# Kernel optimization log

Measured on AMD Instinct MI355X. Metric: run time of the kernel, lower is better.

Reference implementation:

```python
import jax, jax.numpy as jnp
import numpy as np

EPS = 1e-5      # batch-norm epsilon
ALPHA = 0.2     # leaky_relu negative slope


def bn_lrelu(h, gamma, beta):
    # training-mode batch norm over the batch axis, then leaky relu
    mean = jnp.mean(h, axis=0)
    var = jnp.var(h, axis=0)
    h = (h - mean) * jax.lax.rsqrt(var + EPS) * gamma + beta
    return jnp.where(h >= 0, h, ALPHA * h)


def setup_inputs() -> dict:
    key = jax.random.key(0)
    ks = jax.random.split(key, 16)
    O, T, Din, H, Dout = 50000, 200000, 128, 512, 128
    s = 0.02
    inp = {
        "obj_vecs": jax.random.normal(ks[0], (O, Din), jnp.float32),
        "pred_vecs": jax.random.normal(ks[1], (T, Din), jnp.float32),
        "edges": jax.random.randint(ks[2], (T, 2), 0, O, jnp.int64),
        # net1: [3*Din -> H -> 2H+Dout], each Linear followed by BN + leaky_relu
        "W1a": jax.random.normal(ks[3], (3 * Din, H), jnp.float32) * s,
        "b1a": jnp.zeros((H,), jnp.float32),
        "g1a": jnp.ones((H,), jnp.float32),
        "be1a": jnp.zeros((H,), jnp.float32),
        "W1b": jax.random.normal(ks[4], (H, 2 * H + Dout), jnp.float32) * s,
        "b1b": jnp.zeros((2 * H + Dout,), jnp.float32),
        "g1b": jnp.ones((2 * H + Dout,), jnp.float32),
        "be1b": jnp.zeros((2 * H + Dout,), jnp.float32),
        # net2: [H -> H -> Dout]
        "W2a": jax.random.normal(ks[5], (H, H), jnp.float32) * s,
        "b2a": jnp.zeros((H,), jnp.float32),
        "g2a": jnp.ones((H,), jnp.float32),
        "be2a": jnp.zeros((H,), jnp.float32),
        "W2b": jax.random.normal(ks[6], (H, Dout), jnp.float32) * s,
        "b2b": jnp.zeros((Dout,), jnp.float32),
        "g2b": jnp.ones((Dout,), jnp.float32),
        "be2b": jnp.zeros((Dout,), jnp.float32),
    }
    return inp


def reference(obj_vecs, pred_vecs, edges,
              W1a, b1a, g1a, be1a, W1b, b1b, g1b, be1b,
              W2a, b2a, g2a, be2a, W2b, b2b, g2b, be2b):
    O = obj_vecs.shape[0]
    H = W1a.shape[1]
    Dout = W2b.shape[1]
    s_idx = edges[:, 0]
    o_idx = edges[:, 1]

    # gather subject/object vecs and concat with predicate vecs: [T, 3*Din]
    cur_t = jnp.concatenate([obj_vecs[s_idx], pred_vecs, obj_vecs[o_idx]], axis=1)

    # net1 MLP
    h = bn_lrelu(cur_t @ W1a + b1a, g1a, be1a)           # [T, H]
    new_t = bn_lrelu(h @ W1b + b1b, g1b, be1b)            # [T, 2H+Dout]

    new_s = new_t[:, :H]
    new_p = new_t[:, H:H + Dout]
    new_o = new_t[:, H + Dout:]

    # scatter-add pooling back to objects, then average
    pooled = jnp.zeros((O, H), jnp.float32).at[s_idx].add(new_s).at[o_idx].add(new_o)
    counts = jnp.zeros((O,), jnp.float32).at[s_idx].add(1.0).at[o_idx].add(1.0)
    counts = jnp.clip(counts, 1.0, float(O))
    pooled = pooled / counts[:, None]

    # net2 MLP
    h2 = bn_lrelu(pooled @ W2a + b2a, g2a, be2a)          # [O, H]
    new_obj = bn_lrelu(h2 @ W2b + b2b, g2b, be2b)         # [O, Dout]
    return new_obj, new_p
```

## Files before the change

kernel.cpp:

```cpp
#include <hip/hip_runtime.h>

typedef __bf16 bf16;
typedef __bf16 bf16x8 __attribute__((ext_vector_type(8)));
typedef float  f32x4  __attribute__((ext_vector_type(4)));

#define BM 128
#define BN 128
#define BKT 64
#define LDK (BKT + 8)

template<int AMODE, int EPI>
__global__ __launch_bounds__(256) void gemm_k(
    const bf16* __restrict__ Abf, const float* __restrict__ Af32,
    const float* __restrict__ obj, const float* __restrict__ pred,
    const int* __restrict__ edges, const float* __restrict__ invcnt,
    const float* __restrict__ scale, const float* __restrict__ shift,
    const float* __restrict__ oscale, const float* __restrict__ oshift,
    const bf16* __restrict__ WT,
    bf16* __restrict__ outB, float* __restrict__ outF,
    float* __restrict__ pooled, float* __restrict__ gsum, float* __restrict__ gsq,
    int M, int N, int K)
{
  __shared__ __align__(16) bf16 As[BM][LDK];
  __shared__ __align__(16) bf16 Bs[BN][LDK];
  __shared__ float sc_sh[512];
  __shared__ float sh_sh[512];
  __shared__ float osc[BN];
  __shared__ float osh[BN];
  __shared__ int eS[BM];
  __shared__ int eO[BM];

  const int tid = threadIdx.x;
  const int m0 = blockIdx.x * BM;
  const int n0 = blockIdx.y * BN;
  const int lane = tid & 63;
  const int w = tid >> 6;
  const int wm = (w >> 1) * 64;
  const int wn = (w & 1) * 64;
  const int l15 = lane & 15;
  const int quad = lane >> 4;

  if (AMODE == 1) {
    for (int c = tid; c < K; c += 256) { sc_sh[c] = scale[c]; sh_sh[c] = shift[c]; }
  }
  if (EPI == 2) {
    if (tid < BN) { osc[tid] = oscale[n0 + tid]; osh[tid] = oshift[n0 + tid]; }
  }
  if (AMODE == 0 || EPI == 2) {
    if (tid < BM) {
      int r = m0 + tid; if (r >= M) r = M - 1;
      eS[tid] = edges[2 * r];
      eO[tid] = edges[2 * r + 1];
    }
  }
  __syncthreads();

  f32x4 acc[4][4];
  #pragma unroll
  for (int i = 0; i < 4; ++i)
    #pragma unroll
    for (int j = 0; j < 4; ++j)
      acc[i][j] = (f32x4){0.f, 0.f, 0.f, 0.f};

  for (int k0 = 0; k0 < K; k0 += BKT) {
    {
      int idx = tid;
      #pragma unroll
      for (int it = 0; it < 4; ++it, idx += 256) {
        int r = idx >> 3, c8 = (idx & 7) << 3;
        bf16x8 v = *reinterpret_cast<const bf16x8*>(WT + (size_t)(n0 + r) * K + k0 + c8);
        *reinterpret_cast<bf16x8*>(&Bs[r][c8]) = v;
      }
    }
    if (AMODE == 1) {
      int idx = tid;
      #pragma unroll
      for (int it = 0; it < 4; ++it, idx += 256) {
        int r = idx >> 3, c8 = (idx & 7) << 3;
        int row = m0 + r; if (row >= M) row = M - 1;
        bf16x8 v = *reinterpret_cast<const bf16x8*>(Abf + (size_t)row * K + k0 + c8);
        bf16x8 o;
        #pragma unroll
        for (int e = 0; e < 8; ++e) {
          int c = k0 + c8 + e;
          float f = sc_sh[c] * (float)v[e] + sh_sh[c];
          f = f >= 0.f ? f : 0.2f * f;
          o[e] = (bf16)f;
        }
        *reinterpret_cast<bf16x8*>(&As[r][c8]) = o;
      }
    } else {
      int idx = tid;
      #pragma unroll
      for (int it = 0; it < 8; ++it, idx += 256) {
        int r = idx >> 4, c4 = (idx & 15) << 2;
        int row = m0 + r; if (row >= M) row = M - 1;
        const float* src;
        float mul = 1.f;
        if (AMODE == 0) {
          int k = k0 + c4;
          if (k < 128)      src = obj  + (size_t)eS[r] * 128 + k;
          else if (k < 256) src = pred + (size_t)row * 128 + (k - 128);
          else              src = obj  + (size_t)eO[r] * 128 + (k - 256);
        } else {
          src = Af32 + (size_t)row * K + k0 + c4;
          mul = invcnt[row];
        }
        float4 v = *reinterpret_cast<const float4*>(src);
        As[r][c4 + 0] = (bf16)(v.x * mul);
        As[r][c4 + 1] = (bf16)(v.y * mul);
        As[r][c4 + 2] = (bf16)(v.z * mul);
        As[r][c4 + 3] = (bf16)(v.w * mul);
      }
    }
    __syncthreads();
    #pragma unroll
    for (int kk = 0; kk < BKT; kk += 32) {
      bf16x8 af[4], bfv[4];
      #pragma unroll
      for (int i = 0; i < 4; ++i)
        af[i] = *reinterpret_cast<const bf16x8*>(&As[wm + i * 16 + l15][kk + quad * 8]);
      #pragma unroll
      for (int j = 0; j < 4; ++j)
        bfv[j] = *reinterpret_cast<const bf16x8*>(&Bs[wn + j * 16 + l15][kk + quad * 8]);
      #pragma unroll
      for (int i = 0; i < 4; ++i)
        #pragma unroll
        for (int j = 0; j < 4; ++j)
          acc[i][j] = __builtin_amdgcn_mfma_f32_16x16x32_bf16(af[i], bfv[j], acc[i][j], 0, 0, 0);
    }
    __syncthreads();
  }

  if (EPI == 2) {
    #pragma unroll
    for (int i = 0; i < 4; ++i) {
      #pragma unroll
      for (int r = 0; r < 4; ++r) {
        int lrow = wm + i * 16 + quad * 4 + r;
        int row = m0 + lrow;
        if (row >= M) continue;
        #pragma unroll
        for (int j = 0; j < 4; ++j) {
          int cl = wn + j * 16 + l15;
          int n1 = n0 + cl;
          float v = osc[cl] * acc[i][j][r] + osh[cl];
          v = v >= 0.f ? v : 0.2f * v;
          if (n1 < 512)      atomicAdd(&pooled[(size_t)eS[lrow] * 512 + n1], v);
          else if (n1 < 640) outF[(size_t)row * 128 + (n1 - 512)] = v;
          else               atomicAdd(&pooled[(size_t)eO[lrow] * 512 + (n1 - 640)], v);
        }
      }
    }
  } else {
    #pragma unroll
    for (int j = 0; j < 4; ++j) {
      float s = 0.f, q = 0.f;
      #pragma unroll
      for (int i = 0; i < 4; ++i) {
        #pragma unroll
        for (int r = 0; r < 4; ++r) {
          int row = m0 + wm + i * 16 + quad * 4 + r;
          if (row >= M) continue;
          float v = acc[i][j][r];
          s += v; q += v * v;
          int col = n0 + wn + j * 16 + l15;
          if (EPI == 0) outB[(size_t)row * N + col] = (bf16)v;
          if (EPI == 3) outF[(size_t)row * N + col] = v;
        }
      }
      s += __shfl_xor(s, 16); q += __shfl_xor(q, 16);
      s += __shfl_xor(s, 32); q += __shfl_xor(q, 32);
      if (quad == 0) {
        int col = n0 + wn + j * 16 + l15;
        atomicAdd(&gsum[col], s);
        atomicAdd(&gsq[col], q);
      }
    }
  }
}

__global__ __launch_bounds__(256) void tconv_k(const float* __restrict__ W,
                                               bf16* __restrict__ WT, int K, int N) {
  int idx = blockIdx.x * 256 + threadIdx.x;
  if (idx < K * N) {
    int n = idx / K, k = idx - n * K;
    WT[(size_t)n * K + k] = (bf16)W[(size_t)k * N + n];
  }
}

__global__ __launch_bounds__(256) void bnfin_k(const float* __restrict__ sum,
    const float* __restrict__ sq, const float* __restrict__ g,
    const float* __restrict__ be, float* __restrict__ scale,
    float* __restrict__ shift, int C, float invR) {
  int c = blockIdx.x * 256 + threadIdx.x;
  if (c < C) {
    float m = sum[c] * invR;
    float v = sq[c] * invR - m * m;
    float a = g[c] * rsqrtf(v + 1e-5f);
    scale[c] = a;
    shift[c] = be[c] - m * a;
  }
}

__global__ __launch_bounds__(256) void counts_k(const int* __restrict__ edges,
                                                float* __restrict__ counts, int T) {
  int t = blockIdx.x * 256 + threadIdx.x;
  if (t < T) {
    atomicAdd(&counts[edges[2 * t]], 1.f);
    atomicAdd(&counts[edges[2 * t + 1]], 1.f);
  }
}

__global__ __launch_bounds__(256) void invcnt_k(float* __restrict__ counts, int O) {
  int i = blockIdx.x * 256 + threadIdx.x;
  if (i < O) {
    float c = counts[i];
    c = fminf(fmaxf(c, 1.f), (float)O);
    counts[i] = 1.f / c;
  }
}

__global__ __launch_bounds__(256) void final_k(float* __restrict__ buf,
    const float* __restrict__ scale, const float* __restrict__ shift, int n) {
  int i = blockIdx.x * 256 + threadIdx.x;
  if (i < n) {
    int c = i & 127;
    float v = scale[c] * buf[i] + shift[c];
    buf[i] = v >= 0.f ? v : 0.2f * v;
  }
}

extern "C" void kernel_launch(void* const* d_in, const int* in_sizes, int n_in,
                              void* d_out, int out_size, void* d_ws, size_t ws_size,
                              hipStream_t stream) {
  const float* obj   = (const float*)d_in[0];
  const float* pred  = (const float*)d_in[1];
  const int*   edges = (const int*)d_in[2];
  const float* W1a = (const float*)d_in[3];
  const float* g1a = (const float*)d_in[5];
  const float* be1a= (const float*)d_in[6];
  const float* W1b = (const float*)d_in[7];
  const float* g1b = (const float*)d_in[9];
  const float* be1b= (const float*)d_in[10];
  const float* W2a = (const float*)d_in[11];
  const float* g2a = (const float*)d_in[13];
  const float* be2a= (const float*)d_in[14];
  const float* W2b = (const float*)d_in[15];
  const float* g2b = (const float*)d_in[17];
  const float* be2b= (const float*)d_in[18];

  const int O = in_sizes[0] / 128;
  const int T = in_sizes[1] / 128;
  float* out_obj = (float*)d_out;
  float* out_p   = (float*)d_out + (size_t)O * 128;

  char* base = (char*)d_ws;
  size_t off = 0;
  auto alloc = [&](size_t bytes) { size_t p = off; off += (bytes + 255) & ~(size_t)255; return p; };
  size_t oWT1a = alloc((size_t)384 * 512 * 2);
  size_t oWT1b = alloc((size_t)512 * 1152 * 2);
  size_t oWT2a = alloc((size_t)512 * 512 * 2);
  size_t oWT2b = alloc((size_t)512 * 128 * 2);
  size_t oSums = alloc(4608 * 4);
  size_t oScl  = alloc(4608 * 4);
  size_t oCnt  = alloc((size_t)O * 4);
  size_t oHA   = alloc((size_t)T * 512 * 2);
  size_t oPool = alloc((size_t)O * 512 * 4);

  bf16* WT1a = (bf16*)(base + oWT1a);
  bf16* WT1b = (bf16*)(base + oWT1b);
  bf16* WT2a = (bf16*)(base + oWT2a);
  bf16* WT2b = (bf16*)(base + oWT2b);
  float* sums = (float*)(base + oSums);
  float* sumA = sums,        * sqA = sums + 512;
  float* sumB = sums + 1024, * sqB = sums + 2176;
  float* sumC = sums + 3328, * sqC = sums + 3840;
  float* sumD = sums + 4352, * sqD = sums + 4480;
  float* scl = (float*)(base + oScl);
  float* scaleA = scl,        * shiftA = scl + 512;
  float* scaleB = scl + 1024, * shiftB = scl + 2176;
  float* scaleC = scl + 3328, * shiftC = scl + 3840;
  float* scaleD = scl + 4352, * shiftD = scl + 4480;
  float* counts = (float*)(base + oCnt);
  bf16*  hA = (bf16*)(base + oHA);
  bf16*  h2 = (bf16*)(base + oHA);
  float* pooled = (float*)(base + oPool);
  float* objpre = out_obj;

  hipMemsetAsync(sums, 0, 4608 * 4, stream);
  hipMemsetAsync(counts, 0, (size_t)O * 4, stream);
  hipMemsetAsync(pooled, 0, (size_t)O * 512 * 4, stream);

  tconv_k<<<(384 * 512 + 255) / 256, 256, 0, stream>>>(W1a, WT1a, 384, 512);
  tconv_k<<<(512 * 1152 + 255) / 256, 256, 0, stream>>>(W1b, WT1b, 512, 1152);
  tconv_k<<<(512 * 512 + 255) / 256, 256, 0, stream>>>(W2a, WT2a, 512, 512);
  tconv_k<<<(512 * 128 + 255) / 256, 256, 0, stream>>>(W2b, WT2b, 512, 128);
  counts_k<<<(T + 255) / 256, 256, 0, stream>>>(edges, counts, T);
  invcnt_k<<<(O + 255) / 256, 256, 0, stream>>>(counts, O);

  {
    dim3 g((T + BM - 1) / BM, 512 / BN);
    gemm_k<0, 0><<<g, 256, 0, stream>>>(nullptr, nullptr, obj, pred, edges, nullptr,
        nullptr, nullptr, nullptr, nullptr, WT1a, hA, nullptr, nullptr, sumA, sqA,
        T, 512, 384);
  }
  bnfin_k<<<2, 256, 0, stream>>>(sumA, sqA, g1a, be1a, scaleA, shiftA, 512, 1.f / T);

  {
    dim3 g((T + BM - 1) / BM, 1152 / BN);
    gemm_k<1, 1><<<g, 256, 0, stream>>>(hA, nullptr, nullptr, nullptr, nullptr, nullptr,
        scaleA, shiftA, nullptr, nullptr, WT1b, nullptr, nullptr, nullptr, sumB, sqB,
        T, 1152, 512);
  }
  bnfin_k<<<5, 256, 0, stream>>>(sumB, sqB, g1b, be1b, scaleB, shiftB, 1152, 1.f / T);

  {
    dim3 g((T + BM - 1) / BM, 1152 / BN);
    gemm_k<1, 2><<<g, 256, 0, stream>>>(hA, nullptr, nullptr, nullptr, edges, nullptr,
        scaleA, shiftA, scaleB, shiftB, WT1b, nullptr, out_p, pooled, nullptr, nullptr,
        T, 1152, 512);
  }

  {
    dim3 g((O + BM - 1) / BM, 512 / BN);
    gemm_k<2, 0><<<g, 256, 0, stream>>>(nullptr, pooled, nullptr, nullptr, nullptr, counts,
        nullptr, nullptr, nullptr, nullptr, WT2a, h2, nullptr, nullptr, sumC, sqC,
        O, 512, 512);
  }
  bnfin_k<<<2, 256, 0, stream>>>(sumC, sqC, g2a, be2a, scaleC, shiftC, 512, 1.f / O);

  {
    dim3 g((O + BM - 1) / BM, 128 / BN);
    gemm_k<1, 3><<<g, 256, 0, stream>>>(h2, nullptr, nullptr, nullptr, nullptr, nullptr,
        scaleC, shiftC, nullptr, nullptr, WT2b, nullptr, objpre, nullptr, sumD, sqD,
        O, 128, 512);
  }
  bnfin_k<<<1, 256, 0, stream>>>(sumD, sqD, g2b, be2b, scaleD, shiftD, 128, 1.f / O);

  final_k<<<((size_t)O * 128 + 255) / 256, 256, 0, stream>>>(objpre, scaleD, shiftD,
      (int)((size_t)O * 128));
}
```

Before: 2.208 ms.

## Store pre-BN second GEMM output and replace atomic scatter with CSR gather pooling

Instead of running the 1152-wide net1 second GEMM twice (once for BN stats, once to recompute and atomically scatter into pooled), the GEMM runs once and stores the pre-activation output as bf16. A CSR adjacency is then built with an int count, a single-block scan and a fill pass, and a gather kernel applies BN plus leaky relu and averages the contributions per object into a bf16 pooled buffer. The first BN activation is applied once in place by a standalone kernel. This removes a full large GEMM and the float atomics, at the cost of extra global traffic for the T x 1152 bf16 staging buffer, extra bf16 rounding of pooled, and a fallback path used when the workspace is too small.

```diff
diff --git a/kernel.cpp b/kernel.cpp
--- a/kernel.cpp
+++ b/kernel.cpp
@@ -23,12 +23,12 @@
 {
   __shared__ __align__(16) bf16 As[BM][LDK];
   __shared__ __align__(16) bf16 Bs[BN][LDK];
-  __shared__ float sc_sh[512];
-  __shared__ float sh_sh[512];
-  __shared__ float osc[BN];
-  __shared__ float osh[BN];
-  __shared__ int eS[BM];
-  __shared__ int eO[BM];
+  __shared__ float sc_sh[(AMODE == 1) ? 512 : 1];
+  __shared__ float sh_sh[(AMODE == 1) ? 512 : 1];
+  __shared__ float osc[(EPI == 2) ? BN : 1];
+  __shared__ float osh[(EPI == 2) ? BN : 1];
+  __shared__ int eS[(AMODE == 0 || EPI == 2) ? BM : 1];
+  __shared__ int eO[(AMODE == 0 || EPI == 2) ? BM : 1];
 
   const int tid = threadIdx.x;
   const int m0 = blockIdx.x * BM;
@@ -72,22 +72,26 @@
         *reinterpret_cast<bf16x8*>(&Bs[r][c8]) = v;
       }
     }
-    if (AMODE == 1) {
+    if (AMODE == 1 || AMODE == 3) {
       int idx = tid;
       #pragma unroll
       for (int it = 0; it < 4; ++it, idx += 256) {
         int r = idx >> 3, c8 = (idx & 7) << 3;
         int row = m0 + r; if (row >= M) row = M - 1;
         bf16x8 v = *reinterpret_cast<const bf16x8*>(Abf + (size_t)row * K + k0 + c8);
-        bf16x8 o;
-        #pragma unroll
-        for (int e = 0; e < 8; ++e) {
-          int c = k0 + c8 + e;
-          float f = sc_sh[c] * (float)v[e] + sh_sh[c];
-          f = f >= 0.f ? f : 0.2f * f;
-          o[e] = (bf16)f;
+        if (AMODE == 1) {
+          bf16x8 o;
+          #pragma unroll
+          for (int e = 0; e < 8; ++e) {
+            int c = k0 + c8 + e;
+            float f = sc_sh[c] * (float)v[e] + sh_sh[c];
+            f = f >= 0.f ? f : 0.2f * f;
+            o[e] = (bf16)f;
+          }
+          *reinterpret_cast<bf16x8*>(&As[r][c8]) = o;
+        } else {
+          *reinterpret_cast<bf16x8*>(&As[r][c8]) = v;
         }
-        *reinterpret_cast<bf16x8*>(&As[r][c8]) = o;
       }
     } else {
       int idx = tid;
@@ -203,22 +207,133 @@
   }
 }
 
-__global__ __launch_bounds__(256) void counts_k(const int* __restrict__ edges,
-                                                float* __restrict__ counts, int T) {
+__global__ __launch_bounds__(256) void cntint_k(const int* __restrict__ edges,
+                                                int* __restrict__ cnt, int T) {
   int t = blockIdx.x * 256 + threadIdx.x;
   if (t < T) {
-    atomicAdd(&counts[edges[2 * t]], 1.f);
-    atomicAdd(&counts[edges[2 * t + 1]], 1.f);
-  }
-}
-
-__global__ __launch_bounds__(256) void invcnt_k(float* __restrict__ counts, int O) {
+    atomicAdd(&cnt[edges[2 * t]], 1);
+    atomicAdd(&cnt[edges[2 * t + 1]], 1);
+  }
+}
+
+__global__ __launch_bounds__(256) void invcnt_k(const int* __restrict__ cnt,
+                                                float* __restrict__ invc, int O) {
   int i = blockIdx.x * 256 + threadIdx.x;
   if (i < O) {
-    float c = counts[i];
-    c = fminf(fmaxf(c, 1.f), (float)O);
-    counts[i] = 1.f / c;
-  }
+    float c = fminf(fmaxf((float)cnt[i], 1.f), (float)O);
+    invc[i] = 1.f / c;
+  }
+}
+
+__global__ __launch_bounds__(1024) void scan_k(const int* __restrict__ cnt,
+    int* __restrict__ rowptr, int* __restrict__ head, int O, int total) {
+  __shared__ int sh[1024];
+  const int t = threadIdx.x;
+  const int C = (O + 1023) / 1024;
+  const int i0 = t * C;
+  int s = 0;
+  for (int i = 0; i < C; ++i) { int idx = i0 + i; if (idx < O) s += cnt[idx]; }
+  sh[t] = s;
+  __syncthreads();
+  for (int d = 1; d < 1024; d <<= 1) {
+    int v = (t >= d) ? sh[t - d] : 0;
+    __syncthreads();
+    sh[t] += v;
+    __syncthreads();
+  }
+  int run = (t == 0) ? 0 : sh[t - 1];
+  for (int i = 0; i < C; ++i) {
+    int idx = i0 + i;
+    if (idx < O) { rowptr[idx] = run; head[idx] = run; run += cnt[idx]; }
+  }
+  if (t == 0) rowptr[O] = total;
+}
+
+__global__ __launch_bounds__(256) void fill_k(const int* __restrict__ edges,
+    int* __restrict__ head, int* __restrict__ list, int T) {
+  int t = blockIdx.x * 256 + threadIdx.x;
+  if (t < T) {
+    int s = edges[2 * t];
+    int p = atomicAdd(&head[s], 1);
+    list[p] = t << 1;
+    int o = edges[2 * t + 1];
+    p = atomicAdd(&head[o], 1);
+    list[p] = (t << 1) | 1;
+  }
+}
+
+__global__ __launch_bounds__(256) void act_k(bf16* __restrict__ hA,
+    const float* __restrict__ scale, const float* __restrict__ shift, size_t n8) {
+  size_t i = (size_t)blockIdx.x * 256 + threadIdx.x;
+  if (i < n8) {
+    size_t idx8 = i * 8;
+    int c = (int)(idx8 & 511);
+    bf16x8 v = *reinterpret_cast<const bf16x8*>(hA + idx8);
+    bf16x8 o;
+    #pragma unroll
+    for (int j = 0; j < 8; ++j) {
+      float f = scale[c + j] * (float)v[j] + shift[c + j];
+      f = f >= 0.f ? f : 0.2f * f;
+      o[j] = (bf16)f;
+    }
+    *reinterpret_cast<bf16x8*>(hA + idx8) = o;
+  }
+}
+
+__global__ __launch_bounds__(256) void newp_k(const bf16* __restrict__ tB,
+    const float* __restrict__ scale, const float* __restrict__ shift,
+    float* __restrict__ outP, int T) {
+  int i = blockIdx.x * 256 + threadIdx.x;
+  if (i < T * 128) {
+    int t = i >> 7, c = i & 127;
+    float v = scale[512 + c] * (float)tB[(size_t)t * 1152 + 512 + c] + shift[512 + c];
+    outP[i] = v >= 0.f ? v : 0.2f * v;
+  }
+}
+
+__global__ __launch_bounds__(256) void gather_k(const bf16* __restrict__ tB,
+    const int* __restrict__ rowptr, const int* __restrict__ list,
+    const float* __restrict__ scale, const float* __restrict__ shift,
+    const float* __restrict__ invc, bf16* __restrict__ pooled, int O) {
+  int o = blockIdx.x * 4 + (threadIdx.x >> 6);
+  if (o >= O) return;
+  int lane = threadIdx.x & 63;
+  int c0 = lane * 8;
+  float scS[8], shS[8], scO[8], shO[8];
+  #pragma unroll
+  for (int j = 0; j < 8; ++j) {
+    scS[j] = scale[c0 + j];       shS[j] = shift[c0 + j];
+    scO[j] = scale[640 + c0 + j]; shO[j] = shift[640 + c0 + j];
+  }
+  float acc[8];
+  #pragma unroll
+  for (int j = 0; j < 8; ++j) acc[j] = 0.f;
+  int e0 = rowptr[o], e1 = rowptr[o + 1];
+  for (int e = e0; e < e1; ++e) {
+    int id = list[e];
+    int t = id >> 1;
+    int role = id & 1;
+    const bf16* row = tB + (size_t)t * 1152 + (role ? 640 : 0) + c0;
+    bf16x8 v = *reinterpret_cast<const bf16x8*>(row);
+    if (role) {
+      #pragma unroll
+      for (int j = 0; j < 8; ++j) {
+        float f = scO[j] * (float)v[j] + shO[j];
+        acc[j] += (f >= 0.f ? f : 0.2f * f);
+      }
+    } else {
+      #pragma unroll
+      for (int j = 0; j < 8; ++j) {
+        float f = scS[j] * (float)v[j] + shS[j];
+        acc[j] += (f >= 0.f ? f : 0.2f * f);
+      }
+    }
+  }
+  float ic = invc[o];
+  bf16x8 out;
+  #pragma unroll
+  for (int j = 0; j < 8; ++j) out[j] = (bf16)(acc[j] * ic);
+  *reinterpret_cast<bf16x8*>(pooled + (size_t)o * 512 + c0) = out;
 }
 
 __global__ __launch_bounds__(256) void final_k(float* __restrict__ buf,
@@ -264,9 +379,17 @@
   size_t oWT2b = alloc((size_t)512 * 128 * 2);
   size_t oSums = alloc(4608 * 4);
   size_t oScl  = alloc(4608 * 4);
-  size_t oCnt  = alloc((size_t)O * 4);
+  size_t oCntI = alloc((size_t)O * 4);
+  size_t oInvc = alloc((size_t)O * 4);
+  size_t oRp   = alloc((size_t)(O + 1) * 4);
+  size_t oHead = alloc((size_t)O * 4);
+  size_t oList = alloc((size_t)2 * T * 4);
   size_t oHA   = alloc((size_t)T * 512 * 2);
-  size_t oPool = alloc((size_t)O * 512 * 4);
+  size_t oBig  = off;
+  size_t need_staged = oBig + (((size_t)T * 1152 * 2 + 255) & ~(size_t)255)
+                            + (size_t)O * 512 * 2;
+  size_t need_fb     = oBig + (size_t)O * 512 * 4;
+  const bool staged = (ws_size >= need_staged);
 
   bf16* WT1a = (bf16*)(base + oWT1a);
   bf16* WT1b = (bf16*)(base + oWT1b);
@@ -282,22 +405,31 @@
   float* scaleB = scl + 1024, * shiftB = scl + 2176;
   float* scaleC = scl + 3328, * shiftC = scl + 3840;
   float* scaleD = scl + 4352, * shiftD = scl + 4480;
-  float* counts = (float*)(base + oCnt);
+  int*   cntI = (int*)(base + oCntI);
+  float* invc = (float*)(base + oInvc);
+  int*   rowptr = (int*)(base + oRp);
+  int*   head = (int*)(base + oHead);
+  int*   list = (int*)(base + oList);
   bf16*  hA = (bf16*)(base + oHA);
   bf16*  h2 = (bf16*)(base + oHA);
-  float* pooled = (float*)(base + oPool);
+  bf16*  tB = (bf16*)(base + oBig);
+  bf16*  pooledB = (bf16*)(base + oBig + (((size_t)T * 1152 * 2 + 255) & ~(size_t)255));
+  float* pooledF = (float*)(base + oBig);
   float* objpre = out_obj;
 
   hipMemsetAsync(sums, 0, 4608 * 4, stream);
-  hipMemsetAsync(counts, 0, (size_t)O * 4, stream);
-  hipMemsetAsync(pooled, 0, (size_t)O * 512 * 4, stream);
+  hipMemsetAsync(cntI, 0, (size_t)O * 4, stream);
 
   tconv_k<<<(384 * 512 + 255) / 256, 256, 0, stream>>>(W1a, WT1a, 384, 512);
   tconv_k<<<(512 * 1152 + 255) / 256, 256, 0, stream>>>(W1b, WT1b, 512, 1152);
   tconv_k<<<(512 * 512 + 255) / 256, 256, 0, stream>>>(W2a, WT2a, 512, 512);
   tconv_k<<<(512 * 128 + 255) / 256, 256, 0, stream>>>(W2b, WT2b, 512, 128);
-  counts_k<<<(T + 255) / 256, 256, 0, stream>>>(edges, counts, T);
-  invcnt_k<<<(O + 255) / 256, 256, 0, stream>>>(counts, O);
+  cntint_k<<<(T + 255) / 256, 256, 0, stream>>>(edges, cntI, T);
+  invcnt_k<<<(O + 255) / 256, 256, 0, stream>>>(cntI, invc, O);
+  if (staged) {
+    scan_k<<<1, 1024, 0, stream>>>(cntI, rowptr, head, O, 2 * T);
+    fill_k<<<(T + 255) / 256, 256, 0, stream>>>(edges, head, list, T);
+  }
 
   {
     dim3 g((T + BM - 1) / BM, 512 / BN);
@@ -307,26 +439,49 @@
   }
   bnfin_k<<<2, 256, 0, stream>>>(sumA, sqA, g1a, be1a, scaleA, shiftA, 512, 1.f / T);
 
-  {
-    dim3 g((T + BM - 1) / BM, 1152 / BN);
-    gemm_k<1, 1><<<g, 256, 0, stream>>>(hA, nullptr, nullptr, nullptr, nullptr, nullptr,
-        scaleA, shiftA, nullptr, nullptr, WT1b, nullptr, nullptr, nullptr, sumB, sqB,
-        T, 1152, 512);
-  }
-  bnfin_k<<<5, 256, 0, stream>>>(sumB, sqB, g1b, be1b, scaleB, shiftB, 1152, 1.f / T);
-
-  {
-    dim3 g((T + BM - 1) / BM, 1152 / BN);
-    gemm_k<1, 2><<<g, 256, 0, stream>>>(hA, nullptr, nullptr, nullptr, edges, nullptr,
-        scaleA, shiftA, scaleB, shiftB, WT1b, nullptr, out_p, pooled, nullptr, nullptr,
-        T, 1152, 512);
-  }
-
-  {
-    dim3 g((O + BM - 1) / BM, 512 / BN);
-    gemm_k<2, 0><<<g, 256, 0, stream>>>(nullptr, pooled, nullptr, nullptr, nullptr, counts,
-        nullptr, nullptr, nullptr, nullptr, WT2a, h2, nullptr, nullptr, sumC, sqC,
-        O, 512, 512);
+  act_k<<<(int)(((size_t)T * 512 / 8 + 255) / 256), 256, 0, stream>>>(hA, scaleA, shiftA,
+      (size_t)T * 512 / 8);
+
+  if (staged) {
+    {
+      dim3 g((T + BM - 1) / BM, 1152 / BN);
+      gemm_k<3, 0><<<g, 256, 0, stream>>>(hA, nullptr, nullptr, nullptr, nullptr, nullptr,
+          nullptr, nullptr, nullptr, nullptr, WT1b, tB, nullptr, nullptr, sumB, sqB,
+          T, 1152, 512);
+    }
+    bnfin_k<<<5, 256, 0, stream>>>(sumB, sqB, g1b, be1b, scaleB, shiftB, 1152, 1.f / T);
+
+    newp_k<<<(T * 128 + 255) / 256, 256, 0, stream>>>(tB, scaleB, shiftB, out_p, T);
+    gather_k<<<(O + 3) / 4, 256, 0, stream>>>(tB, rowptr, list, scaleB, shiftB, invc,
+        pooledB, O);
+
+    {
+      dim3 g((O + BM - 1) / BM, 512 / BN);
+      gemm_k<3, 0><<<g, 256, 0, stream>>>(pooledB, nullptr, nullptr, nullptr, nullptr,
+          nullptr, nullptr, nullptr, nullptr, nullptr, WT2a, h2, nullptr, nullptr,
+          sumC, sqC, O, 512, 512);
+    }
+  } else {
+    hipMemsetAsync(pooledF, 0, (size_t)O * 512 * 4, stream);
+    {
+      dim3 g((T + BM - 1) / BM, 1152 / BN);
+      gemm_k<3, 1><<<g, 256, 0, stream>>>(hA, nullptr, nullptr, nullptr, nullptr, nullptr,
+          nullptr, nullptr, nullptr, nullptr, WT1b, nullptr, nullptr, nullptr, sumB, sqB,
+          T, 1152, 512);
+    }
+    bnfin_k<<<5, 256, 0, stream>>>(sumB, sqB, g1b, be1b, scaleB, shiftB, 1152, 1.f / T);
+    {
+      dim3 g((T + BM - 1) / BM, 1152 / BN);
+      gemm_k<3, 2><<<g, 256, 0, stream>>>(hA, nullptr, nullptr, nullptr, edges, nullptr,
+          nullptr, nullptr, scaleB, shiftB, WT1b, nullptr, out_p, pooledF, nullptr,
+          nullptr, T, 1152, 512);
+    }
+    {
+      dim3 g((O + BM - 1) / BM, 512 / BN);
+      gemm_k<2, 0><<<g, 256, 0, stream>>>(nullptr, pooledF, nullptr, nullptr, nullptr,
+          invc, nullptr, nullptr, nullptr, nullptr, WT2a, h2, nullptr, nullptr,
+          sumC, sqC, O, 512, 512);
+    }
   }
   bnfin_k<<<2, 256, 0, stream>>>(sumC, sqC, g2a, be2a, scaleC, shiftC, 512, 1.f / O);
 
```

New measurement: 2.151 ms. -2.6%, faster.
